# Kernel optimization log

Measured on AMD Instinct MI355X. Metric: run time of the kernel, lower is better.

The kernel has to match this reference:

```python
import jax, jax.numpy as jnp
import numpy as np
from jax import lax

# Config matching init_kwargs
H, W = 64, 64
DIM = 160
HEADS = 5
KD = DIM // HEADS            # key_dim = head_dim = 32 (attn_ratio=1 -> d == key_dim)
WS = 14                       # window size -> n = 196 tokens per window
HIDDEN = int(DIM * 4.0)
EPS = 1e-5


def _make_bias_idxs(ws):
    pts = [(i, j) for i in range(ws) for j in range(ws)]
    offs, idxs = {}, []
    for p1 in pts:
        for p2 in pts:
            o = (abs(p1[0] - p2[0]), abs(p1[1] - p2[1]))
            if o not in offs:
                offs[o] = len(offs)
            idxs.append(offs[o])
    n = len(pts)
    return np.asarray(idxs, np.int32).reshape(n, n), len(offs)


def setup_inputs() -> dict:
    key = jax.random.key(0)
    ks = jax.random.split(key, 10)
    bias_idxs_np, n_off = _make_bias_idxs(WS)  # [196,196], 196 unique offsets
    s = 0.02
    return {
        "x": jax.random.normal(ks[0], (16, H * W, DIM), jnp.float32),
        "ln1_g": jnp.ones((DIM,), jnp.float32),
        "ln1_b": jnp.zeros((DIM,), jnp.float32),
        "qkv_w": jax.random.normal(ks[1], (3 * KD * HEADS, DIM), jnp.float32) * s,
        "qkv_b": jnp.zeros((3 * KD * HEADS,), jnp.float32),
        "proj_w": jax.random.normal(ks[2], (DIM, KD * HEADS), jnp.float32) * s,
        "proj_b": jnp.zeros((DIM,), jnp.float32),
        "attn_biases": jax.random.normal(ks[3], (HEADS, n_off), jnp.float32) * s,
        "conv_w": jax.random.normal(ks[4], (DIM, 1, 3, 3), jnp.float32) * s,  # depthwise OIHW
        "bn_g": jnp.ones((DIM,), jnp.float32),
        "bn_b": jnp.zeros((DIM,), jnp.float32),
        "ln2_g": jnp.ones((DIM,), jnp.float32),
        "ln2_b": jnp.zeros((DIM,), jnp.float32),
        "fc1_w": jax.random.normal(ks[5], (HIDDEN, DIM), jnp.float32) * s,
        "fc1_b": jnp.zeros((HIDDEN,), jnp.float32),
        "fc2_w": jax.random.normal(ks[6], (DIM, HIDDEN), jnp.float32) * s,
        "fc2_b": jnp.zeros((DIM,), jnp.float32),
        "bias_idxs": jnp.asarray(bias_idxs_np),
    }


def _layernorm(x, g, b):
    m = jnp.mean(x, -1, keepdims=True)
    v = jnp.mean(jnp.square(x - m), -1, keepdims=True)
    return (x - m) * lax.rsqrt(v + EPS) * g + b


def reference(x, ln1_g, ln1_b, qkv_w, qkv_b, proj_w, proj_b, attn_biases,
              conv_w, bn_g, bn_b, ln2_g, ln2_b, fc1_w, fc1_b, fc2_w, fc2_b,
              bias_idxs):
    b, l, c = x.shape
    res = x
    # ---- window partition (64 -> pad 70 -> 5x5 windows of 14x14 = 196 tokens)
    pad_b = (WS - H % WS) % WS
    pad_r = (WS - W % WS) % WS
    xg = x.reshape(b, H, W, c)
    xg = jnp.pad(xg, ((0, 0), (0, pad_b), (0, pad_r), (0, 0)))
    ph, pw = H + pad_b, W + pad_r
    nh, nw = ph // WS, pw // WS
    n = WS * WS
    xw = xg.reshape(b, nh, WS, nw, WS, c).transpose(0, 1, 3, 2, 4, 5).reshape(b * nh * nw, n, c)
    # ---- attention with gathered relative-position bias
    xn = _layernorm(xw, ln1_g, ln1_b)
    qkv = (xn @ qkv_w.T + qkv_b).reshape(xw.shape[0], n, HEADS, 3 * KD)
    q, k, v = qkv[..., :KD], qkv[..., KD:2 * KD], qkv[..., 2 * KD:]
    bias = attn_biases[:, bias_idxs]  # [HEADS, n, n]
    scores = jnp.einsum('bnhd,bmhd->bhnm', q, k) * (KD ** -0.5) + bias
    a = jax.nn.softmax(scores, axis=-1)
    out = jnp.einsum('bhnm,bmhd->bnhd', a, v).reshape(xw.shape[0], n, HEADS * KD)
    xw = out @ proj_w.T + proj_b
    # ---- window merge + unpad
    xg = xw.reshape(b, nh, nw, WS, WS, c).transpose(0, 1, 3, 2, 4, 5).reshape(b, ph, pw, c)
    xg = xg[:, :H, :W]
    x = res + xg.reshape(b, l, c)
    # ---- depthwise 3x3 conv + BN (eval: running_mean=0, running_var=1)
    xc = x.transpose(0, 2, 1).reshape(b, c, H, W)
    y = lax.conv_general_dilated(xc, conv_w, (1, 1), [(1, 1), (1, 1)],
                                 dimension_numbers=('NCHW', 'OIHW', 'NCHW'),
                                 feature_group_count=c)
    y = y * (bn_g * lax.rsqrt(jnp.float32(1.0 + EPS)))[None, :, None, None] + bn_b[None, :, None, None]
    x = y.reshape(b, c, l).transpose(0, 2, 1)
    # ---- MLP with pre-LN and exact GELU
    xn = _layernorm(x, ln2_g, ln2_b)
    h = jax.nn.gelu(xn @ fc1_w.T + fc1_b, approximate=False)
    m = h @ fc2_w.T + fc2_b
    return x + m
```

## Files before the change

### kernel.cpp

```cpp
#include <hip/hip_runtime.h>
#include <hip/hip_bf16.h>
#include <math.h>

typedef unsigned short ushort;
typedef __attribute__((ext_vector_type(4))) float f32x4;
typedef __attribute__((ext_vector_type(8))) short s16x8;
typedef __attribute__((ext_vector_type(4))) short s16x4;
typedef __attribute__((ext_vector_type(4))) ushort u16x4;

#define H_    64
#define W_    64
#define DIM   160
#define HEADS 5
#define KD    32
#define WS    14
#define NTOK  196
#define NWIN  400
#define HIDDEN 640
#define EPS   1e-5f
#define NROW  (NWIN*NTOK)
#define BATCH 16
#define L_    (H_*W_)
#define MROW  (BATCH*L_)
#define CS    0.25507875861f

#if __has_builtin(__builtin_amdgcn_exp2f)
#define EXP2(x) __builtin_amdgcn_exp2f(x)
#else
#define EXP2(x) exp2f(x)
#endif

__device__ __forceinline__ ushort f2bfbits(float f) {
    unsigned u = __float_as_uint(f);
    unsigned r = (u + 0x7fffu + ((u >> 16) & 1u)) >> 16;
    return (ushort)r;
}

__global__ __launch_bounds__(256) void pre_kernel(
    const float* __restrict__ qkv_w, const float* __restrict__ proj_w,
    const float* __restrict__ fc1_w, const float* __restrict__ fc2_w,
    const float* __restrict__ conv_w, const float* __restrict__ bn_g,
    const float* __restrict__ abias, const int* __restrict__ bidx,
    ushort* __restrict__ wb, float* __restrict__ cwT,
    float* __restrict__ biasP, int n_off)
{
    const int gid = blockIdx.x * 256 + threadIdx.x;
    if (gid < 19200) {
        float4 v = ((const float4*)qkv_w)[gid];
        u16x4 o = { f2bfbits(v.x), f2bfbits(v.y), f2bfbits(v.z), f2bfbits(v.w) };
        *(u16x4*)(wb + gid * 4) = o;
    } else if (gid < 25600) {
        const int i = gid - 19200;
        float4 v = ((const float4*)proj_w)[i];
        u16x4 o = { f2bfbits(v.x), f2bfbits(v.y), f2bfbits(v.z), f2bfbits(v.w) };
        *(u16x4*)(wb + 76800 + i * 4) = o;
    } else if (gid < 38400) {
        const int idx = gid - 25600;
        const int l = idx & 63, rest = idx >> 6;
        const int jj = rest % 5, ht = rest / 5;
        const float* src = fc1_w + (size_t)(ht * 16 + (l & 15)) * 160
                         + jj * 32 + (l >> 4) * 8;
        const float4 v0 = *(const float4*)src;
        const float4 v1 = *(const float4*)(src + 4);
        u16x4 o0 = { f2bfbits(v0.x), f2bfbits(v0.y), f2bfbits(v0.z), f2bfbits(v0.w) };
        u16x4 o1 = { f2bfbits(v1.x), f2bfbits(v1.y), f2bfbits(v1.z), f2bfbits(v1.w) };
        *(u16x4*)(wb + 102400 + idx * 8)     = o0;
        *(u16x4*)(wb + 102400 + idx * 8 + 4) = o1;
    } else if (gid < 51200) {
        const int idx = gid - 38400;
        const int l = idx & 63, f = idx >> 6;
        const int dt = f % 10, u = f / 10;
        const float* base = fc2_w + (size_t)(dt * 16 + (l & 15)) * HIDDEN
                          + u * 32 + 4 * (l >> 4);
        const float4 v0 = *(const float4*)base;
        const float4 v1 = *(const float4*)(base + 16);
        u16x4 o0 = { f2bfbits(v0.x), f2bfbits(v0.y), f2bfbits(v0.z), f2bfbits(v0.w) };
        u16x4 o1 = { f2bfbits(v1.x), f2bfbits(v1.y), f2bfbits(v1.z), f2bfbits(v1.w) };
        *(u16x4*)(wb + 204800 + idx * 8)     = o0;
        *(u16x4*)(wb + 204800 + idx * 8 + 4) = o1;
    } else if (gid < 51560) {
        const int i = gid - 51200;
        const int t = i / 40, c4 = (i % 40) * 4;
#pragma unroll
        for (int j = 0; j < 4; ++j) {
            const int c = c4 + j;
            cwT[t * DIM + c] = conv_w[c * 9 + t] * bn_g[c] * rsqrtf(1.0f + EPS);
        }
    } else if (gid < 267880) {
        const int idx = gid - 51560;
        const int ln = idx & 255, f = idx >> 8;
        const int h = f / 169, rem = f % 169;
        const int qt = rem / 13, kt = rem % 13;
        int q = qt * 16 + (ln & 15); if (q > NTOK - 1) q = NTOK - 1;
        const int k0 = kt * 16 + (ln >> 4) * 4;
        float4 o;
        float* ov = (float*)&o;
#pragma unroll
        for (int r = 0; r < 4; ++r) {
            const int k = k0 + r;
            ov[r] = (k < NTOK)
                ? abias[h * n_off + bidx[q * NTOK + k]] * 1.4426950408889634f
                : 0.f;
        }
        *(float4*)(biasP + (size_t)idx * 4) = o;
    }
}

__global__ __launch_bounds__(256) void ln1_win_kernel(
    const float* __restrict__ x, const float* __restrict__ g,
    const float* __restrict__ b, ushort* __restrict__ xn)
{
    const int row = blockIdx.x * 4 + (threadIdx.x >> 6);
    const int win = row / NTOK, tok = row % NTOK;
    const int bb = win / 25, wr = (win % 25) / 5, wc = win % 5;
    const int gh = wr * WS + tok / WS, gw = wc * WS + tok % WS;
    const bool valid = (gh < H_) && (gw < W_);
    const float* xrow = x + ((size_t)bb * L_ + (size_t)gh * W_ + gw) * DIM;
    const int lane = threadIdx.x & 63;
    float v0 = 0.f, v1 = 0.f, v2 = 0.f;
    if (valid) {
        v0 = xrow[lane];
        v1 = xrow[lane + 64];
        if (lane < 32) v2 = xrow[lane + 128];
    }
    float s  = v0 + v1 + v2;
    float sq = v0 * v0 + v1 * v1 + v2 * v2;
#pragma unroll
    for (int off = 32; off; off >>= 1) { s += __shfl_xor(s, off); sq += __shfl_xor(sq, off); }
    const float mean = s * (1.0f / DIM);
    const float var  = sq * (1.0f / DIM) - mean * mean;
    const float rs   = rsqrtf(var + EPS);
    ushort* orow = xn + (size_t)row * DIM;
    orow[lane]      = f2bfbits((v0 - mean) * rs * g[lane]      + b[lane]);
    orow[lane + 64] = f2bfbits((v1 - mean) * rs * g[lane + 64] + b[lane + 64]);
    if (lane < 32) orow[lane + 128] = f2bfbits((v2 - mean) * rs * g[lane + 128] + b[lane + 128]);
}

template <int EPI>
__global__ __launch_bounds__(512) void gemm_mfma(
    const ushort* __restrict__ A, const ushort* __restrict__ Wb,
    const float* __restrict__ bias, void* __restrict__ Cv,
    const float* __restrict__ extra, int M, int N)
{
    __shared__ ushort Bs[160][164];
    const int tid = threadIdx.x;
    const int wv = tid >> 6, ln = tid & 63;
    const int g = ln >> 4, l15 = ln & 15;
    const int wvm = wv & 3, wvn = wv >> 2;
    const int m0 = blockIdx.y * 128, n0 = blockIdx.x * 160;

    for (int e = tid; e < 160 * 20; e += 512) {
        const int row = e / 20, part = e % 20;
        *(int4*)&Bs[row][part * 8] =
            *(const int4*)(Wb + (size_t)(n0 + row) * 160 + part * 8);
    }

    s16x8 a[2][5];
#pragma unroll
    for (int mt = 0; mt < 2; ++mt) {
        int am = m0 + wvm * 32 + mt * 16 + l15; if (am >= M) am = M - 1;
        const ushort* ap = A + (size_t)am * 160 + g * 8;
#pragma unroll
        for (int s = 0; s < 5; ++s) a[mt][s] = *(const s16x8*)(ap + s * 32);
    }
    __syncthreads();

    f32x4 acc[2][5] = {};
#pragma unroll
    for (int j = 0; j < 5; ++j) {
#pragma unroll
        for (int nt = 0; nt < 5; ++nt) {
            const s16x8 bf = *(const s16x8*)&Bs[wvn * 80 + nt * 16 + l15][j * 32 + g * 8];
            acc[0][nt] = __builtin_amdgcn_mfma_f32_16x16x32_bf16(a[0][j], bf, acc[0][nt], 0, 0, 0);
            acc[1][nt] = __builtin_amdgcn_mfma_f32_16x16x32_bf16(a[1][j], bf, acc[1][nt], 0, 0, 0);
        }
    }

#pragma unroll
    for (int mt = 0; mt < 2; ++mt) {
#pragma unroll
        for (int nt = 0; nt < 5; ++nt) {
            const int n = n0 + wvn * 80 + nt * 16 + l15;
            const float bn = bias[n];
#pragma unroll
            for (int r = 0; r < 4; ++r) {
                const int m = m0 + wvm * 32 + mt * 16 + g * 4 + r;
                if (m >= M) continue;
                float val = acc[mt][nt][r] + bn;
                if (EPI == 0) {
                    if ((n % 96) < 32) val *= CS;
                    ((ushort*)Cv)[(size_t)m * N + n] = f2bfbits(val);
                } else {
                    const int win = m / NTOK, tok = m % NTOK;
                    const int bb = win / 25, wr = (win % 25) / 5, wc = win % 5;
                    const int gh = wr * WS + tok / WS, gw = wc * WS + tok % WS;
                    if (gh < H_ && gw < W_) {
                        const size_t off = ((size_t)bb * L_ + (size_t)gh * W_ + gw) * DIM + n;
                        ((float*)Cv)[off] = extra[off] + val;
                    }
                }
            }
        }
    }
}

__global__ __launch_bounds__(256, 3) void mlp_fused(
    float* xo, const ushort* __restrict__ w1p, const ushort* __restrict__ w2p,
    const float* __restrict__ fc1_b, const float* __restrict__ fc2_b,
    const float* __restrict__ lng, const float* __restrict__ lnb)
{
    __shared__ ushort W1s[10240];
    __shared__ ushort W2s[10240];
    const int tid = threadIdx.x;
    const int wv = tid >> 6, ln = tid & 63;
    const int g = ln >> 4, l15 = ln & 15;
    const int row0 = blockIdx.x * 64 + wv * 16;

    const float* xp = xo + (size_t)(row0 + l15) * DIM + g * 8;
    float4 va[10];
    float vsum = 0.f, vsq = 0.f;
#pragma unroll
    for (int s = 0; s < 5; ++s) {
        const float4 p0 = *(const float4*)(xp + s * 32);
        const float4 p1 = *(const float4*)(xp + s * 32 + 4);
        va[s * 2] = p0; va[s * 2 + 1] = p1;
        vsum += (p0.x + p0.y) + (p0.z + p0.w) + (p1.x + p1.y) + (p1.z + p1.w);
        vsq  += (p0.x*p0.x + p0.y*p0.y) + (p0.z*p0.z + p0.w*p0.w)
              + (p1.x*p1.x + p1.y*p1.y) + (p1.z*p1.z + p1.w*p1.w);
    }
    vsum += __shfl_xor(vsum, 16); vsum += __shfl_xor(vsum, 32);
    vsq  += __shfl_xor(vsq, 16);  vsq  += __shfl_xor(vsq, 32);
    const float mean = vsum * (1.0f / DIM);
    const float rs = rsqrtf(vsq * (1.0f / DIM) - mean * mean + EPS);
    s16x8 a1[5];
#pragma unroll
    for (int s = 0; s < 5; ++s) {
        const float4 g0 = *(const float4*)(lng + s * 32 + g * 8);
        const float4 g1 = *(const float4*)(lng + s * 32 + g * 8 + 4);
        const float4 bb0 = *(const float4*)(lnb + s * 32 + g * 8);
        const float4 bb1 = *(const float4*)(lnb + s * 32 + g * 8 + 4);
        const float4 p0 = va[s * 2], p1 = va[s * 2 + 1];
        ushort o[8];
        o[0] = f2bfbits((p0.x - mean) * rs * g0.x + bb0.x);
        o[1] = f2bfbits((p0.y - mean) * rs * g0.y + bb0.y);
        o[2] = f2bfbits((p0.z - mean) * rs * g0.z + bb0.z);
        o[3] = f2bfbits((p0.w - mean) * rs * g0.w + bb0.w);
        o[4] = f2bfbits((p1.x - mean) * rs * g1.x + bb1.x);
        o[5] = f2bfbits((p1.y - mean) * rs * g1.y + bb1.y);
        o[6] = f2bfbits((p1.z - mean) * rs * g1.z + bb1.z);
        o[7] = f2bfbits((p1.w - mean) * rs * g1.w + bb1.w);
        a1[s] = *(const s16x8*)o;
    }

    f32x4 oacc[10] = {};
    for (int c = 0; c < 10; ++c) {
        if (c) __syncthreads();
        const ushort* s1 = w1p + c * 10240;
        const ushort* s2 = w2p + c * 10240;
        for (int e = tid; e < 1280; e += 256) {
            *(int4*)&W1s[e * 8] = *(const int4*)(s1 + e * 8);
            *(int4*)&W2s[e * 8] = *(const int4*)(s2 + e * 8);
        }
        __syncthreads();

#pragma unroll
        for (int p = 0; p < 2; ++p) {
            f32x4 h0 = {0.f,0.f,0.f,0.f}, h1 = {0.f,0.f,0.f,0.f};
#pragma unroll
            for (int jj = 0; jj < 5; ++jj) {
                const s16x8 wfe = *(const s16x8*)&W1s[(((p * 2) * 5 + jj) * 64 + ln) * 8];
                const s16x8 wfo = *(const s16x8*)&W1s[(((p * 2 + 1) * 5 + jj) * 64 + ln) * 8];
                h0 = __builtin_amdgcn_mfma_f32_16x16x32_bf16(wfe, a1[jj], h0, 0, 0, 0);
                h1 = __builtin_amdgcn_mfma_f32_16x16x32_bf16(wfo, a1[jj], h1, 0, 0, 0);
            }
            const int hb0 = c * 64 + p * 32 + g * 4;
            const float4 hbe = *(const float4*)(fc1_b + hb0);
            const float4 hbo = *(const float4*)(fc1_b + hb0 + 16);
            const float hbev[4] = { hbe.x, hbe.y, hbe.z, hbe.w };
            const float hbov[4] = { hbo.x, hbo.y, hbo.z, hbo.w };
            ushort pk[8];
#pragma unroll
            for (int r = 0; r < 4; ++r) {
                float v = h0[r] + hbev[r];
                float t = EXP2(-2.302259756f * fmaf(0.044715f * v * v, v, v));
                pk[r] = f2bfbits(v * __builtin_amdgcn_rcpf(1.0f + t));
                v = h1[r] + hbov[r];
                t = EXP2(-2.302259756f * fmaf(0.044715f * v * v, v, v));
                pk[4 + r] = f2bfbits(v * __builtin_amdgcn_rcpf(1.0f + t));
            }
            const s16x8 P = *(const s16x8*)pk;
#pragma unroll
            for (int dt = 0; dt < 10; ++dt) {
                const s16x8 w2f = *(const s16x8*)&W2s[((p * 10 + dt) * 64 + ln) * 8];
                oacc[dt] = __builtin_amdgcn_mfma_f32_16x16x32_bf16(P, w2f, oacc[dt], 0, 0, 0);
            }
        }
    }

#pragma unroll
    for (int dt = 0; dt < 10; ++dt) {
        const float bn = fc2_b[dt * 16 + l15];
#pragma unroll
        for (int r = 0; r < 4; ++r) {
            const size_t off = (size_t)(row0 + g * 4 + r) * DIM + dt * 16 + l15;
            xo[off] += oacc[dt][r] + bn;
        }
    }
}

__global__ __launch_bounds__(256) void attn_mfma_kernel(
    const ushort* __restrict__ qkv, const float* __restrict__ biasP,
    ushort* __restrict__ out)
{
    __shared__ ushort Ks[208][40];
    __shared__ ushort VT[32][212];
    const int win = blockIdx.x / HEADS;
    const int h   = blockIdx.x % HEADS;
    const int tid = threadIdx.x;
    const size_t base = (size_t)win * NTOK;
    const ushort* qbase = qkv + base * 480 + h * 96;

    for (int e = tid; e < 208 * 4; e += 256) {
        const int row = e >> 2, part = e & 3;
        const int gr = row < NTOK ? row : NTOK - 1;
        *(int4*)&Ks[row][part * 8] = *(const int4*)(qbase + (size_t)gr * 480 + 32 + part * 8);
    }
    for (int e = tid; e < NTOK * 4; e += 256) {
        const int key = e >> 2, part = e & 3;
        int4 p = *(const int4*)(qbase + (size_t)key * 480 + 64 + part * 8);
        const ushort* u = (const ushort*)&p;
#pragma unroll
        for (int j = 0; j < 8; ++j) VT[part * 8 + j][key] = u[j];
    }
    for (int e = tid; e < 12 * 32; e += 256) VT[e & 31][NTOK + (e >> 5)] = 0;
    __syncthreads();

    const int wv = tid >> 6, ln = tid & 63, g = ln >> 4, l15 = ln & 15;

    for (int qt = wv; qt < 13; qt += 4) {
        const int qr = qt * 16 + l15;
        const int qc = qr < NTOK ? qr : NTOK - 1;
        const s16x8 qf = *(const s16x8*)(qbase + (size_t)qc * 480 + g * 8);
        const float* bq = biasP + ((size_t)(h * 13 + qt) * 13) * 1024;

        f32x4 S[13];
#pragma unroll
        for (int kt = 0; kt < 13; ++kt)
            S[kt] = *(const f32x4*)(bq + kt * 1024 + ln * 4);
#pragma unroll
        for (int kt = 0; kt < 13; ++kt) {
            const s16x8 kf = *(const s16x8*)&Ks[kt * 16 + l15][g * 8];
            S[kt] = __builtin_amdgcn_mfma_f32_16x16x32_bf16(kf, qf, S[kt], 0, 0, 0);
        }
        float mx = -1e30f;
#pragma unroll
        for (int kt = 0; kt < 13; ++kt) {
#pragma unroll
            for (int r = 0; r < 4; ++r) {
                if (kt == 12) {
                    const int key = 192 + g * 4 + r;
                    if (key >= NTOK) S[kt][r] = -1e30f;
                }
                mx = fmaxf(mx, S[kt][r]);
            }
        }
        mx = fmaxf(mx, __shfl_xor(mx, 16));
        mx = fmaxf(mx, __shfl_xor(mx, 32));

        float sum = 0.f;
        s16x4 P[13];
#pragma unroll
        for (int kt = 0; kt < 13; ++kt) {
            const float p0 = EXP2(S[kt][0] - mx);
            const float p1 = EXP2(S[kt][1] - mx);
            const float p2 = EXP2(S[kt][2] - mx);
            const float p3 = EXP2(S[kt][3] - mx);
            sum += (p0 + p1) + (p2 + p3);
            P[kt] = (s16x4){ (short)f2bfbits(p0), (short)f2bfbits(p1),
                             (short)f2bfbits(p2), (short)f2bfbits(p3) };
        }
        sum += __shfl_xor(sum, 16);
        sum += __shfl_xor(sum, 32);

        f32x4 o0 = {0.f,0.f,0.f,0.f}, o1 = {0.f,0.f,0.f,0.f};
#pragma unroll
        for (int kt = 0; kt < 13; ++kt) {
            const s16x4 vf0 = *(const s16x4*)&VT[l15][kt * 16 + g * 4];
            const s16x4 vf1 = *(const s16x4*)&VT[16 + l15][kt * 16 + g * 4];
            o0 = __builtin_amdgcn_mfma_f32_16x16x16bf16_1k(vf0, P[kt], o0, 0, 0, 0);
            o1 = __builtin_amdgcn_mfma_f32_16x16x16bf16_1k(vf1, P[kt], o1, 0, 0, 0);
        }
        if (qr < NTOK) {
            const float inv = 1.0f / sum;
            ushort* op = out + (base + qr) * DIM + h * KD;
            u16x4 w0 = { f2bfbits(o0[0] * inv), f2bfbits(o0[1] * inv),
                         f2bfbits(o0[2] * inv), f2bfbits(o0[3] * inv) };
            u16x4 w1 = { f2bfbits(o1[0] * inv), f2bfbits(o1[1] * inv),
                         f2bfbits(o1[2] * inv), f2bfbits(o1[3] * inv) };
            *(u16x4*)(op + g * 4)      = w0;
            *(u16x4*)(op + 16 + g * 4) = w1;
        }
    }
}

__global__ __launch_bounds__(256) void dwconv_bn_kernel(
    const float* __restrict__ xin, const float* __restrict__ cwT,
    const float* __restrict__ bnb, float* __restrict__ xout)
{
    const int gid = blockIdx.x * 256 + threadIdx.x;
    const int pos = gid / 40, c4 = (gid % 40) * 4;
    const int bb = pos >> 12, hw = pos & 4095;
    const int hh = hw >> 6, ww = hw & 63;
    float4 acc = *(const float4*)&bnb[c4];
#pragma unroll
    for (int kh = -1; kh <= 1; ++kh) {
        const int ih = hh + kh;
        if (ih < 0 || ih >= H_) continue;
#pragma unroll
        for (int kw = -1; kw <= 1; ++kw) {
            const int iw = ww + kw;
            if (iw < 0 || iw >= W_) continue;
            const float4 xv = *(const float4*)&xin[((size_t)(bb << 12) + (ih << 6) + iw) * DIM + c4];
            const float4 wv = *(const float4*)&cwT[((kh + 1) * 3 + (kw + 1)) * DIM + c4];
            acc.x = fmaf(xv.x, wv.x, acc.x);
            acc.y = fmaf(xv.y, wv.y, acc.y);
            acc.z = fmaf(xv.z, wv.z, acc.z);
            acc.w = fmaf(xv.w, wv.w, acc.w);
        }
    }
    *(float4*)&xout[(size_t)pos * DIM + c4] = acc;
}

extern "C" void kernel_launch(void* const* d_in, const int* in_sizes, int n_in,
                              void* d_out, int out_size, void* d_ws, size_t ws_size,
                              hipStream_t stream)
{
    const float* x      = (const float*)d_in[0];
    const float* ln1_g  = (const float*)d_in[1];
    const float* ln1_b  = (const float*)d_in[2];
    const float* qkv_w  = (const float*)d_in[3];
    const float* qkv_b  = (const float*)d_in[4];
    const float* proj_w = (const float*)d_in[5];
    const float* proj_b = (const float*)d_in[6];
    const float* abias  = (const float*)d_in[7];
    const float* conv_w = (const float*)d_in[8];
    const float* bn_g   = (const float*)d_in[9];
    const float* bn_b   = (const float*)d_in[10];
    const float* ln2_g  = (const float*)d_in[11];
    const float* ln2_b  = (const float*)d_in[12];
    const float* fc1_w  = (const float*)d_in[13];
    const float* fc1_b  = (const float*)d_in[14];
    const float* fc2_w  = (const float*)d_in[15];
    const float* fc2_b  = (const float*)d_in[16];
    const int*   bidx   = (const int*)d_in[17];
    const int    n_off  = in_sizes[7] / HEADS;

    char* ws = (char*)d_ws;
    ushort* xn    = (ushort*)(ws);
    ushort* qkv   = (ushort*)(ws + 25088000);
    ushort* ao    = (ushort*)(ws + 100352000);
    float*  biasP = (float*)(ws + 125440000);
    float*  x1    = (float*)(ws + 125440000);
    ushort* wb    = (ushort*)(ws + 167383040);
    float*  cwT   = (float*)(ws + 167997440);
    float*  x2    = (float*)d_out;

    pre_kernel<<<dim3(1047), dim3(256), 0, stream>>>(
        qkv_w, proj_w, fc1_w, fc2_w, conv_w, bn_g, abias, bidx, wb, cwT, biasP, n_off);

    ln1_win_kernel<<<dim3(NROW / 4), dim3(256), 0, stream>>>(x, ln1_g, ln1_b, xn);

    gemm_mfma<0><<<dim3(3, 613), dim3(512), 0, stream>>>(
        xn, wb, qkv_b, (void*)qkv, nullptr, NROW, 480);

    attn_mfma_kernel<<<dim3(NWIN * HEADS), dim3(256), 0, stream>>>(qkv, biasP, ao);

    gemm_mfma<1><<<dim3(1, 613), dim3(512), 0, stream>>>(
        ao, wb + 76800, proj_b, (void*)x1, x, NROW, 160);

    dwconv_bn_kernel<<<dim3(MROW * 40 / 256), dim3(256), 0, stream>>>(
        x1, cwT, bn_b, x2);

    mlp_fused<<<dim3(MROW / 64), dim3(256), 0, stream>>>(
        x2, wb + 102400, wb + 204800, fc1_b, fc2_b, ln2_g, ln2_b);
}
```

Baseline: 255.7 us.

## Process multiple M strips per GEMM block with prefetch and vectorized epilogue

```diff
diff --git a/kernel.cpp b/kernel.cpp
--- a/kernel.cpp
+++ b/kernel.cpp
@@ -23,6 +23,7 @@
 #define L_    (H_*W_)
 #define MROW  (BATCH*L_)
 #define CS    0.25507875861f
+#define GSTRIPS 4
 
 #if __has_builtin(__builtin_amdgcn_exp2f)
 #define EXP2(x) __builtin_amdgcn_exp2f(x)
@@ -147,7 +148,8 @@
     const int wv = tid >> 6, ln = tid & 63;
     const int g = ln >> 4, l15 = ln & 15;
     const int wvm = wv & 3, wvn = wv >> 2;
-    const int m0 = blockIdx.y * 128, n0 = blockIdx.x * 160;
+    const int n0 = blockIdx.y * 160;
+    const int strip0 = blockIdx.x * GSTRIPS;
 
     for (int e = tid; e < 160 * 20; e += 512) {
         const int row = e / 20, part = e % 20;
@@ -156,47 +158,79 @@
     }
 
     s16x8 a[2][5];
-#pragma unroll
-    for (int mt = 0; mt < 2; ++mt) {
-        int am = m0 + wvm * 32 + mt * 16 + l15; if (am >= M) am = M - 1;
-        const ushort* ap = A + (size_t)am * 160 + g * 8;
-#pragma unroll
-        for (int s = 0; s < 5; ++s) a[mt][s] = *(const s16x8*)(ap + s * 32);
+    {
+        const int m0 = strip0 * 128;
+#pragma unroll
+        for (int mt = 0; mt < 2; ++mt) {
+            int am = m0 + wvm * 32 + mt * 16 + l15; if (am >= M) am = M - 1;
+            const ushort* ap = A + (size_t)am * 160 + g * 8;
+#pragma unroll
+            for (int s = 0; s < 5; ++s) a[mt][s] = *(const s16x8*)(ap + s * 32);
+        }
     }
     __syncthreads();
 
-    f32x4 acc[2][5] = {};
-#pragma unroll
-    for (int j = 0; j < 5; ++j) {
-#pragma unroll
-        for (int nt = 0; nt < 5; ++nt) {
-            const s16x8 bf = *(const s16x8*)&Bs[wvn * 80 + nt * 16 + l15][j * 32 + g * 8];
-            acc[0][nt] = __builtin_amdgcn_mfma_f32_16x16x32_bf16(a[0][j], bf, acc[0][nt], 0, 0, 0);
-            acc[1][nt] = __builtin_amdgcn_mfma_f32_16x16x32_bf16(a[1][j], bf, acc[1][nt], 0, 0, 0);
-        }
-    }
-
-#pragma unroll
-    for (int mt = 0; mt < 2; ++mt) {
-#pragma unroll
-        for (int nt = 0; nt < 5; ++nt) {
-            const int n = n0 + wvn * 80 + nt * 16 + l15;
-            const float bn = bias[n];
-#pragma unroll
-            for (int r = 0; r < 4; ++r) {
-                const int m = m0 + wvm * 32 + mt * 16 + g * 4 + r;
-                if (m >= M) continue;
-                float val = acc[mt][nt][r] + bn;
-                if (EPI == 0) {
-                    if ((n % 96) < 32) val *= CS;
-                    ((ushort*)Cv)[(size_t)m * N + n] = f2bfbits(val);
-                } else {
-                    const int win = m / NTOK, tok = m % NTOK;
-                    const int bb = win / 25, wr = (win % 25) / 5, wc = win % 5;
-                    const int gh = wr * WS + tok / WS, gw = wc * WS + tok % WS;
-                    if (gh < H_ && gw < W_) {
-                        const size_t off = ((size_t)bb * L_ + (size_t)gh * W_ + gw) * DIM + n;
-                        ((float*)Cv)[off] = extra[off] + val;
+    for (int s = 0; s < GSTRIPS; ++s) {
+        const int m0 = (strip0 + s) * 128;
+        if (m0 >= M) break;
+
+        f32x4 acc[2][5] = {};
+#pragma unroll
+        for (int j = 0; j < 5; ++j) {
+#pragma unroll
+            for (int nt = 0; nt < 5; ++nt) {
+                const s16x8 bf = *(const s16x8*)&Bs[wvn * 80 + nt * 16 + l15][j * 32 + g * 8];
+                acc[0][nt] = __builtin_amdgcn_mfma_f32_16x16x32_bf16(bf, a[0][j], acc[0][nt], 0, 0, 0);
+                acc[1][nt] = __builtin_amdgcn_mfma_f32_16x16x32_bf16(bf, a[1][j], acc[1][nt], 0, 0, 0);
+            }
+        }
+
+        if (s + 1 < GSTRIPS) {
+            const int mn = (strip0 + s + 1) * 128;
+#pragma unroll
+            for (int mt = 0; mt < 2; ++mt) {
+                int am = mn + wvm * 32 + mt * 16 + l15; if (am >= M) am = M - 1;
+                const ushort* ap = A + (size_t)am * 160 + g * 8;
+#pragma unroll
+                for (int jj = 0; jj < 5; ++jj) a[mt][jj] = *(const s16x8*)(ap + jj * 32);
+            }
+        }
+
+#pragma unroll
+        for (int mt = 0; mt < 2; ++mt) {
+            const int m = m0 + wvm * 32 + mt * 16 + l15;
+            if (m >= M) continue;
+            if (EPI == 0) {
+                ushort* orow = (ushort*)Cv + (size_t)m * N;
+#pragma unroll
+                for (int nt = 0; nt < 5; ++nt) {
+                    const int n = n0 + wvn * 80 + nt * 16 + g * 4;
+                    const float4 bn = *(const float4*)&bias[n];
+                    const float sc = ((n % 96) < 32) ? CS : 1.0f;
+                    u16x4 o = { f2bfbits((acc[mt][nt][0] + bn.x) * sc),
+                                f2bfbits((acc[mt][nt][1] + bn.y) * sc),
+                                f2bfbits((acc[mt][nt][2] + bn.z) * sc),
+                                f2bfbits((acc[mt][nt][3] + bn.w) * sc) };
+                    *(u16x4*)(orow + n) = o;
+                }
+            } else {
+                const int win = m / NTOK, tok = m % NTOK;
+                const int bb = win / 25, wr = (win % 25) / 5, wc = win % 5;
+                const int gh = wr * WS + tok / WS, gw = wc * WS + tok % WS;
+                if (gh < H_ && gw < W_) {
+                    const size_t rowoff = ((size_t)bb * L_ + (size_t)gh * W_ + gw) * DIM;
+                    float* orow = (float*)Cv + rowoff;
+                    const float* erow = extra + rowoff;
+#pragma unroll
+                    for (int nt = 0; nt < 5; ++nt) {
+                        const int n = n0 + wvn * 80 + nt * 16 + g * 4;
+                        const float4 bn = *(const float4*)&bias[n];
+                        const float4 res = *(const float4*)&erow[n];
+                        float4 o4 = { res.x + acc[mt][nt][0] + bn.x,
+                                      res.y + acc[mt][nt][1] + bn.y,
+                                      res.z + acc[mt][nt][2] + bn.z,
+                                      res.w + acc[mt][nt][3] + bn.w };
+                        *(float4*)&orow[n] = o4;
                     }
                 }
             }
@@ -465,17 +499,19 @@
     float*  cwT   = (float*)(ws + 167997440);
     float*  x2    = (float*)d_out;
 
+    const int mblocks = (NROW + 128 * GSTRIPS - 1) / (128 * GSTRIPS);
+
     pre_kernel<<<dim3(1047), dim3(256), 0, stream>>>(
         qkv_w, proj_w, fc1_w, fc2_w, conv_w, bn_g, abias, bidx, wb, cwT, biasP, n_off);
 
     ln1_win_kernel<<<dim3(NROW / 4), dim3(256), 0, stream>>>(x, ln1_g, ln1_b, xn);
 
-    gemm_mfma<0><<<dim3(3, 613), dim3(512), 0, stream>>>(
+    gemm_mfma<0><<<dim3(mblocks, 3), dim3(512), 0, stream>>>(
         xn, wb, qkv_b, (void*)qkv, nullptr, NROW, 480);
 
     attn_mfma_kernel<<<dim3(NWIN * HEADS), dim3(256), 0, stream>>>(qkv, biasP, ao);
 
-    gemm_mfma<1><<<dim3(1, 613), dim3(512), 0, stream>>>(
+    gemm_mfma<1><<<dim3(mblocks, 1), dim3(512), 0, stream>>>(
         ao, wb + 76800, proj_b, (void*)x1, x, NROW, 160);
 
     dwconv_bn_kernel<<<dim3(MROW * 40 / 256), dim3(256), 0, stream>>>(
```

Result: faster. 237.1 us (-7.2%).
